# Kernel tuning notes

Measured on AMD Instinct MI355X. Metric: run time of the kernel, lower is better.

## Reference

```python
import jax, jax.numpy as jnp
import numpy as np

N_EXPERTS = 8
TOP_K = 2
W_SCALE = 0.02


def setup_inputs() -> dict:
    key = jax.random.key(0)
    ks = jax.random.split(key, 4)
    S, B, D, F = 2048, 2, 1024, 4096
    x = jax.random.normal(ks[0], (S, B, D), dtype=jnp.float32)
    gate_w = jax.random.normal(ks[1], (D, N_EXPERTS), dtype=jnp.float32) * W_SCALE
    gate_b = jnp.zeros((N_EXPERTS,), dtype=jnp.float32)
    w1 = jax.random.normal(ks[2], (N_EXPERTS, D, F), dtype=jnp.float32) * W_SCALE
    b1 = jnp.zeros((N_EXPERTS, F), dtype=jnp.float32)
    w2 = jax.random.normal(ks[3], (N_EXPERTS, F, D), dtype=jnp.float32) * W_SCALE
    b2 = jnp.zeros((N_EXPERTS, D), dtype=jnp.float32)
    return {"x": x, "gate_w": gate_w, "gate_b": gate_b,
            "w1": w1, "b1": b1, "w2": w2, "b2": b2}


def reference(x, gate_w, gate_b, w1, b1, w2, b2):
    # gate logits: [S, B, E]
    logits = jnp.einsum('sbd,de->sbe', x, gate_w) + gate_b
    top_w, top_idx = jax.lax.top_k(logits, TOP_K)            # [S,B,K]
    # softmax over the top-k logits in float32 (matches dtype=torch.float)
    probs = jax.nn.softmax(top_w.astype(jnp.float32), axis=-1)
    # dense combine weights [S, B, E]: zero for non-selected experts
    comb = jnp.sum(jax.nn.one_hot(top_idx, N_EXPERTS, dtype=probs.dtype)
                   * probs[..., None], axis=-2)
    out = jnp.zeros_like(x)
    for e in range(N_EXPERTS):  # fixed small structural loop over experts
        h = jax.nn.relu(jnp.einsum('sbd,df->sbf', x, w1[e]) + b1[e])
        y = jnp.einsum('sbf,fd->sbd', h, w2[e]) + b2[e]
        out = out + comb[..., e:e + 1].astype(x.dtype) * y
    return out
```

## Files before the change

kernel.cpp:

```cpp
#include <hip/hip_runtime.h>
#include <stdint.h>

#define T_TOK 4096
#define D_DIM 1024
#define F_DIM 4096
#define NEXP 8
#define BM 128
#define BN 128
#define BK 32
#define CAP 9216
#define MT_MAX (CAP / BM)

typedef __attribute__((ext_vector_type(8))) short short8;
typedef __attribute__((ext_vector_type(4))) float f4;
typedef __attribute__((ext_vector_type(4))) unsigned short us4;

#define WS_SBASE   64
#define WS_TBASE   96
#define WS_TOPI    256
#define WS_TOPP    (WS_TOPI + T_TOK*2*4)
#define WS_PSLOT   (WS_TOPP + T_TOK*2*4)
#define WS_XG      102400
#define WS_H       (WS_XG + (size_t)CAP*D_DIM*2)
#define WS_Y       (WS_H + (size_t)CAP*F_DIM*2)
#define WS_WT      (WS_Y + (size_t)CAP*D_DIM*2)

__device__ __forceinline__ unsigned short f2bf(float f) {
    union { float f; uint32_t u; } c; c.f = f;
    uint32_t r = c.u + 0x7FFFu + ((c.u >> 16) & 1u);
    return (unsigned short)(r >> 16);
}
__device__ __forceinline__ float bf2f(unsigned short h) {
    union { uint32_t u; float f; } c; c.u = ((uint32_t)h) << 16;
    return c.f;
}

__global__ __launch_bounds__(256) void gate_kernel(
    const float* __restrict__ x, const float* __restrict__ gw,
    const float* __restrict__ gb,
    int* __restrict__ top_idx, float* __restrict__ top_p)
{
    int lane = threadIdx.x & 63;
    int t = blockIdx.x * 4 + (threadIdx.x >> 6);
    const float* xr = x + (size_t)t * D_DIM;
    float acc[8] = {0.f,0.f,0.f,0.f,0.f,0.f,0.f,0.f};
    for (int i = 0; i < 16; ++i) {
        int d = lane + i * 64;
        float xv = xr[d];
        const float* g = gw + d * 8;
        #pragma unroll
        for (int e = 0; e < 8; ++e) acc[e] += xv * g[e];
    }
    #pragma unroll
    for (int e = 0; e < 8; ++e) {
        #pragma unroll
        for (int off = 32; off > 0; off >>= 1)
            acc[e] += __shfl_xor(acc[e], off, 64);
    }
    if (lane == 0) {
        float l[8];
        #pragma unroll
        for (int e = 0; e < 8; ++e) l[e] = acc[e] + gb[e];
        int i0 = 0; float m0 = l[0];
        #pragma unroll
        for (int e = 1; e < 8; ++e) if (l[e] > m0) { m0 = l[e]; i0 = e; }
        int i1 = -1; float m1 = -3.4e38f;
        #pragma unroll
        for (int e = 0; e < 8; ++e) if (e != i0 && l[e] > m1) { m1 = l[e]; i1 = e; }
        float p0 = 1.f / (1.f + expf(m1 - m0));
        top_idx[t*2]   = i0; top_idx[t*2+1] = i1;
        top_p[t*2]     = p0; top_p[t*2+1]   = 1.f - p0;
    }
}

__global__ __launch_bounds__(256) void plan_kernel(
    const int* __restrict__ top_idx, int* __restrict__ sbase,
    int* __restrict__ tbase, int* __restrict__ pslot)
{
    __shared__ int woff[4][8];
    __shared__ int sb_s[8];
    int t = threadIdx.x, wv = t >> 6, lane = t & 63;
    int base = t * 32;

    int h[8] = {0,0,0,0,0,0,0,0};
    for (int i = 0; i < 32; ++i) {
        int e = top_idx[base + i];
        #pragma unroll
        for (int ee = 0; ee < 8; ++ee) h[ee] += (e == ee) ? 1 : 0;
    }
    int inc[8];
    #pragma unroll
    for (int ee = 0; ee < 8; ++ee) {
        int v = h[ee];
        #pragma unroll
        for (int off = 1; off < 64; off <<= 1) {
            int n = __shfl_up(v, off, 64);
            if (lane >= off) v += n;
        }
        inc[ee] = v;
    }
    if (lane == 63) {
        #pragma unroll
        for (int ee = 0; ee < 8; ++ee) woff[wv][ee] = inc[ee];
    }
    __syncthreads();
    if (t == 0) {
        int cnt[8];
        #pragma unroll
        for (int ee = 0; ee < 8; ++ee) {
            int s = 0;
            #pragma unroll
            for (int w = 0; w < 4; ++w) { int v = woff[w][ee]; woff[w][ee] = s; s += v; }
            cnt[ee] = s;
        }
        int b = 0, tb0 = 0;
        tbase[0] = 0;
        #pragma unroll
        for (int e = 0; e < 8; ++e) {
            sb_s[e] = b; sbase[e] = b;
            int mt = (cnt[e] + BM - 1) / BM;
            b += mt * BM; tb0 += mt;
            tbase[e + 1] = tb0;
        }
    }
    __syncthreads();
    int run[8];
    #pragma unroll
    for (int ee = 0; ee < 8; ++ee)
        run[ee] = sb_s[ee] + woff[wv][ee] + inc[ee] - h[ee];
    for (int i = 0; i < 32; ++i) {
        int e = top_idx[base + i];
        int slot = 0;
        #pragma unroll
        for (int ee = 0; ee < 8; ++ee) slot += (e == ee) ? run[ee] : 0;
        pslot[base + i] = slot;
        #pragma unroll
        for (int ee = 0; ee < 8; ++ee) run[ee] += (e == ee) ? 1 : 0;
    }
}

__global__ __launch_bounds__(256) void gather_kernel(
    const float* __restrict__ x, const int* __restrict__ pslot,
    uint16_t* __restrict__ xg)
{
    int t = blockIdx.x;
    int s0 = pslot[2*t], s1 = pslot[2*t + 1];
    int i = threadIdx.x;
    f4 v = ((const f4*)(x + (size_t)t * D_DIM))[i];
    us4 o;
    o.x = f2bf(v[0]); o.y = f2bf(v[1]); o.z = f2bf(v[2]); o.w = f2bf(v[3]);
    *(us4*)(xg + (size_t)s0 * D_DIM + i * 4) = o;
    *(us4*)(xg + (size_t)s1 * D_DIM + i * 4) = o;
}

__global__ __launch_bounds__(512) void convT_kernel(
    const float* __restrict__ W, uint16_t* __restrict__ WT, int K, int N)
{
    __shared__ float ts[64][65];
    int e = blockIdx.z;
    int n0 = blockIdx.x * 64, k0 = blockIdx.y * 64;
    const float* src = W + (size_t)e * K * N + (size_t)k0 * N + n0;
    int t = threadIdx.x;
    int kk = t >> 3, j = t & 7;
    f4 v0 = *(const f4*)(src + (size_t)kk * N + j * 8);
    f4 v1 = *(const f4*)(src + (size_t)kk * N + j * 8 + 4);
    #pragma unroll
    for (int i = 0; i < 4; ++i) ts[j*8 + i][kk] = v0[i];
    #pragma unroll
    for (int i = 0; i < 4; ++i) ts[j*8 + 4 + i][kk] = v1[i];
    __syncthreads();
    int nn = t >> 3;
    short8 o;
    #pragma unroll
    for (int i = 0; i < 8; ++i) o[i] = (short)f2bf(ts[nn][j*8 + i]);
    *(short8*)(WT + (size_t)e * N * K + (size_t)(n0 + nn) * K + k0 + j * 8) = o;
}

template<bool RELU>
__global__ __launch_bounds__(256, 3) void moe_gemm3(
    const uint16_t* __restrict__ A, const uint16_t* __restrict__ Bt,
    const float* __restrict__ bias, uint16_t* __restrict__ Cc,
    const int* __restrict__ tbase, const int* __restrict__ sbase,
    int K, int N, int NT)
{
    __shared__ uint16_t As3[3][BM][BK];
    __shared__ uint16_t Bs3[3][BN][BK];

    int nwg = gridDim.x;
    int lin = blockIdx.x;
    int wg = (lin & 7) * (nwg >> 3) + (lin >> 3);
    int q = wg >> 2;
    int nt = q % NT;
    int mt = (wg & 3) + (q / NT) * 4;

    if (mt >= tbase[8]) return;
    int e = 0;
    while (mt >= tbase[e + 1]) ++e;
    int row0 = sbase[e] + (mt - tbase[e]) * BM;
    int n0 = nt * BN;
    const uint16_t* Be = Bt + (size_t)e * N * K + (size_t)n0 * K;

    int tid = threadIdx.x;
    int wid = tid >> 6, lane = tid & 63;
    int wrow = (wid >> 1) * 64, wcol = (wid & 1) * 64;

    f4 acc[4][4] = {};

    int ovb = tid * 16;
    int rowA[2], koffA[2];
    #pragma unroll
    for (int j = 0; j < 2; ++j) {
        int ov = ovb + j * 4096;
        int row = ov >> 6;
        int cb  = (ov >> 4) & 3;
        rowA[j]  = row;
        koffA[j] = (cb ^ ((row >> 1) & 3)) << 3;
    }

    int abyte[4], bbyte[4];
    #pragma unroll
    for (int m = 0; m < 4; ++m) {
        int r = wrow + m * 16 + (lane & 15);
        abyte[m] = r * 64 + ((((lane >> 4) ^ ((r >> 1) & 3))) << 4);
    }
    #pragma unroll
    for (int n = 0; n < 4; ++n) {
        int c = wcol + n * 16 + (lane & 15);
        bbyte[n] = c * 64 + ((((lane >> 4) ^ ((c >> 1) & 3))) << 4);
    }
    const char* As0 = (const char*)&As3[0][0][0];
    const char* Bs0 = (const char*)&Bs3[0][0][0];

    auto STAGE = [&](int buf, int kt) {
        #pragma unroll
        for (int j = 0; j < 2; ++j) {
            const uint16_t* gpA = A + (size_t)(row0 + rowA[j]) * K + kt + koffA[j];
            __builtin_amdgcn_global_load_lds(
                (const __attribute__((address_space(1))) void*)gpA,
                (__attribute__((address_space(3))) void*)((char*)&As3[buf][0][0] + ovb + j * 4096),
                16, 0, 0);
            const uint16_t* gpB = Be + (size_t)rowA[j] * K + kt + koffA[j];
            __builtin_amdgcn_global_load_lds(
                (const __attribute__((address_space(1))) void*)gpB,
                (__attribute__((address_space(3))) void*)((char*)&Bs3[buf][0][0] + ovb + j * 4096),
                16, 0, 0);
        }
    };

    int nkt = K / BK;
    STAGE(0, 0);
    STAGE(1, BK);
    asm volatile("s_waitcnt vmcnt(4)" ::: "memory");
    __builtin_amdgcn_s_barrier();

    int buf = 0;
    for (int t = 0; t < nkt; ++t) {
        int cb = buf * 8192;
        short8 af[4], bfr[4];
        #pragma unroll
        for (int m = 0; m < 4; ++m) af[m] = *(const short8*)(As0 + cb + abyte[m]);
        #pragma unroll
        for (int n = 0; n < 4; ++n) bfr[n] = *(const short8*)(Bs0 + cb + bbyte[n]);

        bool stg = (t + 2) < nkt;
        if (stg) {
            int b2 = buf + 2; if (b2 >= 3) b2 -= 3;
            STAGE(b2, (t + 2) * BK);
        }

        #pragma unroll
        for (int m = 0; m < 4; ++m)
            #pragma unroll
            for (int n = 0; n < 4; ++n)
                acc[m][n] = __builtin_amdgcn_mfma_f32_16x16x32_bf16(
                    af[m], bfr[n], acc[m][n], 0, 0, 0);

        if (stg) asm volatile("s_waitcnt vmcnt(4)" ::: "memory");
        else     asm volatile("s_waitcnt vmcnt(0)" ::: "memory");
        __builtin_amdgcn_s_barrier();
        buf = (buf + 1 == 3) ? 0 : buf + 1;
    }

    #pragma unroll
    for (int n = 0; n < 4; ++n) {
        int c = wcol + n * 16 + (lane & 15);
        float bv = bias[(size_t)e * N + n0 + c];
        #pragma unroll
        for (int m = 0; m < 4; ++m) {
            int rb = wrow + m * 16 + (lane >> 4) * 4;
            #pragma unroll
            for (int r = 0; r < 4; ++r) {
                float v = acc[m][n][r] + bv;
                if (RELU) v = fmaxf(v, 0.f);
                Cc[(size_t)(row0 + rb + r) * N + n0 + c] = f2bf(v);
            }
        }
    }
}

__global__ __launch_bounds__(256) void combine_kernel(
    const uint16_t* __restrict__ Y, const int* __restrict__ pair_slot,
    const float* __restrict__ top_p, float* __restrict__ out)
{
    int t = blockIdx.x;
    int s0 = pair_slot[t*2], s1 = pair_slot[t*2+1];
    float p0 = top_p[t*2],  p1 = top_p[t*2+1];
    int i = threadIdx.x * 4;
    us4 a = *(const us4*)(Y + (size_t)s0 * D_DIM + i);
    us4 b = *(const us4*)(Y + (size_t)s1 * D_DIM + i);
    f4 o;
    o[0] = p0 * bf2f(a.x) + p1 * bf2f(b.x);
    o[1] = p0 * bf2f(a.y) + p1 * bf2f(b.y);
    o[2] = p0 * bf2f(a.z) + p1 * bf2f(b.z);
    o[3] = p0 * bf2f(a.w) + p1 * bf2f(b.w);
    *(f4*)(out + (size_t)t * D_DIM + i) = o;
}

extern "C" void kernel_launch(void* const* d_in, const int* in_sizes, int n_in,
                              void* d_out, int out_size, void* d_ws, size_t ws_size,
                              hipStream_t stream)
{
    const float* x  = (const float*)d_in[0];
    const float* gw = (const float*)d_in[1];
    const float* gb = (const float*)d_in[2];
    const float* w1 = (const float*)d_in[3];
    const float* b1 = (const float*)d_in[4];
    const float* w2 = (const float*)d_in[5];
    const float* b2 = (const float*)d_in[6];
    float* out = (float*)d_out;

    char* ws = (char*)d_ws;
    int*   sbase = (int*)(ws + WS_SBASE);
    int*   tbase = (int*)(ws + WS_TBASE);
    int*   topi  = (int*)(ws + WS_TOPI);
    float* topp  = (float*)(ws + WS_TOPP);
    int*   pslot = (int*)(ws + WS_PSLOT);
    uint16_t* xg = (uint16_t*)(ws + WS_XG);
    uint16_t* H  = (uint16_t*)(ws + WS_H);
    uint16_t* Y  = (uint16_t*)(ws + WS_Y);
    uint16_t* WT = (uint16_t*)(ws + WS_WT);

    gate_kernel<<<T_TOK / 4, 256, 0, stream>>>(x, gw, gb, topi, topp);
    plan_kernel<<<1, 256, 0, stream>>>(topi, sbase, tbase, pslot);
    gather_kernel<<<T_TOK, 256, 0, stream>>>(x, pslot, xg);

    convT_kernel<<<dim3(F_DIM/64, D_DIM/64, NEXP), 512, 0, stream>>>(w1, WT, D_DIM, F_DIM);
    moe_gemm3<true ><<<MT_MAX * (F_DIM / BN), 256, 0, stream>>>(
        xg, WT, b1, H, tbase, sbase, D_DIM, F_DIM, F_DIM / BN);
    convT_kernel<<<dim3(D_DIM/64, F_DIM/64, NEXP), 512, 0, stream>>>(w2, WT, F_DIM, D_DIM);
    moe_gemm3<false><<<MT_MAX * (D_DIM / BN), 256, 0, stream>>>(
        H, WT, b2, Y, tbase, sbase, F_DIM, D_DIM, D_DIM / BN);

    combine_kernel<<<T_TOK, 256, 0, stream>>>(Y, pslot, topp, out);
}
```

Baseline: 299.1 us.

## Use 256-row tiles for first expert GEMM and reuse gather buffer for Y

Adds a new moe_gemm5 kernel with 256x128 output tiles (8x4 MFMA accumulators per wave) for the up-projection, so each weight tile loaded into LDS is reused across twice as many rows. The plan kernel now pads each expert's rows to a multiple of 256 and emits separate tile bases for the 256- and 128-row GEMMs. Capacity grows, and Y aliases the xg buffer to save workspace. The larger tiles raise register and LDS pressure and add padding waste per expert.

```diff
diff --git a/kernel.cpp b/kernel.cpp
--- a/kernel.cpp
+++ b/kernel.cpp
@@ -8,8 +8,9 @@
 #define BM 128
 #define BN 128
 #define BK 32
-#define CAP 9216
-#define MT_MAX (CAP / BM)
+#define CAP 10240
+#define MT256 (CAP / 256)
+#define MT128 (CAP / 128)
 
 typedef __attribute__((ext_vector_type(8))) short short8;
 typedef __attribute__((ext_vector_type(4))) float f4;
@@ -17,13 +18,13 @@
 
 #define WS_SBASE   64
 #define WS_TBASE   96
+#define WS_TB128   160
 #define WS_TOPI    256
 #define WS_TOPP    (WS_TOPI + T_TOK*2*4)
 #define WS_PSLOT   (WS_TOPP + T_TOK*2*4)
 #define WS_XG      102400
 #define WS_H       (WS_XG + (size_t)CAP*D_DIM*2)
-#define WS_Y       (WS_H + (size_t)CAP*F_DIM*2)
-#define WS_WT      (WS_Y + (size_t)CAP*D_DIM*2)
+#define WS_WT      (WS_H + (size_t)CAP*F_DIM*2)
 
 __device__ __forceinline__ unsigned short f2bf(float f) {
     union { float f; uint32_t u; } c; c.f = f;
@@ -75,7 +76,8 @@
 
 __global__ __launch_bounds__(256) void plan_kernel(
     const int* __restrict__ top_idx, int* __restrict__ sbase,
-    int* __restrict__ tbase, int* __restrict__ pslot)
+    int* __restrict__ tbase256, int* __restrict__ tbase128,
+    int* __restrict__ pslot)
 {
     __shared__ int woff[4][8];
     __shared__ int sb_s[8];
@@ -113,14 +115,17 @@
             for (int w = 0; w < 4; ++w) { int v = woff[w][ee]; woff[w][ee] = s; s += v; }
             cnt[ee] = s;
         }
-        int b = 0, tb0 = 0;
-        tbase[0] = 0;
+        int b = 0, t2 = 0, t1 = 0;
+        tbase256[0] = 0; tbase128[0] = 0;
         #pragma unroll
         for (int e = 0; e < 8; ++e) {
             sb_s[e] = b; sbase[e] = b;
-            int mt = (cnt[e] + BM - 1) / BM;
-            b += mt * BM; tb0 += mt;
-            tbase[e + 1] = tb0;
+            int m2 = (cnt[e] + 255) / 256;
+            b  += m2 * 256;
+            t2 += m2;
+            t1 += m2 * 2;
+            tbase256[e + 1] = t2;
+            tbase128[e + 1] = t1;
         }
     }
     __syncthreads();
@@ -288,6 +293,132 @@
         #pragma unroll
         for (int m = 0; m < 4; ++m) {
             int rb = wrow + m * 16 + (lane >> 4) * 4;
+            #pragma unroll
+            for (int r = 0; r < 4; ++r) {
+                float v = acc[m][n][r] + bv;
+                if (RELU) v = fmaxf(v, 0.f);
+                Cc[(size_t)(row0 + rb + r) * N + n0 + c] = f2bf(v);
+            }
+        }
+    }
+}
+
+template<bool RELU>
+__global__ __launch_bounds__(256, 2) void moe_gemm5(
+    const uint16_t* __restrict__ A, const uint16_t* __restrict__ Bt,
+    const float* __restrict__ bias, uint16_t* __restrict__ Cc,
+    const int* __restrict__ tbase, const int* __restrict__ sbase,
+    int K, int N, int NT)
+{
+    __shared__ uint16_t As3[3][256][BK];
+    __shared__ uint16_t Bs3[3][BN][BK];
+
+    int nwg = gridDim.x;
+    int lin = blockIdx.x;
+    int wg = (lin & 7) * (nwg >> 3) + (lin >> 3);
+    int q = wg >> 2;
+    int nt = q % NT;
+    int mt = (wg & 3) + (q / NT) * 4;
+
+    if (mt >= tbase[8]) return;
+    int e = 0;
+    while (mt >= tbase[e + 1]) ++e;
+    int row0 = sbase[e] + (mt - tbase[e]) * 256;
+    int n0 = nt * BN;
+    const uint16_t* Be = Bt + (size_t)e * N * K + (size_t)n0 * K;
+
+    int tid = threadIdx.x;
+    int wid = tid >> 6, lane = tid & 63;
+    int wr = wid >> 1, wc = wid & 1;
+    int lq = lane >> 4, lr = lane & 15;
+
+    f4 acc[8][4] = {};
+
+    int ovb = tid * 16;
+    int rowS[4], koffS[4];
+    #pragma unroll
+    for (int j = 0; j < 4; ++j) {
+        int ov = ovb + j * 4096;
+        int row = ov >> 6;
+        int cb  = (ov >> 4) & 3;
+        rowS[j]  = row;
+        koffS[j] = (cb ^ ((row >> 1) & 3)) << 3;
+    }
+
+    int abyte[8], bbyte[4];
+    #pragma unroll
+    for (int m = 0; m < 8; ++m) {
+        int r = wr * 128 + m * 16 + lr;
+        abyte[m] = r * 64 + (((lq ^ ((r >> 1) & 3))) << 4);
+    }
+    #pragma unroll
+    for (int n = 0; n < 4; ++n) {
+        int c = wc * 64 + n * 16 + lr;
+        bbyte[n] = c * 64 + (((lq ^ ((c >> 1) & 3))) << 4);
+    }
+    const char* As0 = (const char*)&As3[0][0][0];
+    const char* Bs0 = (const char*)&Bs3[0][0][0];
+
+    auto STAGE = [&](int buf, int kt) {
+        #pragma unroll
+        for (int j = 0; j < 4; ++j) {
+            const uint16_t* gpA = A + (size_t)(row0 + rowS[j]) * K + kt + koffS[j];
+            __builtin_amdgcn_global_load_lds(
+                (const __attribute__((address_space(1))) void*)gpA,
+                (__attribute__((address_space(3))) void*)((char*)&As3[buf][0][0] + ovb + j * 4096),
+                16, 0, 0);
+        }
+        #pragma unroll
+        for (int j = 0; j < 2; ++j) {
+            const uint16_t* gpB = Be + (size_t)rowS[j] * K + kt + koffS[j];
+            __builtin_amdgcn_global_load_lds(
+                (const __attribute__((address_space(1))) void*)gpB,
+                (__attribute__((address_space(3))) void*)((char*)&Bs3[buf][0][0] + ovb + j * 4096),
+                16, 0, 0);
+        }
+    };
+
+    int nkt = K / BK;
+    STAGE(0, 0);
+    STAGE(1, BK);
+    asm volatile("s_waitcnt vmcnt(6)" ::: "memory");
+    __builtin_amdgcn_s_barrier();
+
+    int buf = 0;
+    for (int t = 0; t < nkt; ++t) {
+        int cba = buf * 16384, cbb = buf * 8192;
+        short8 af[8], bfr[4];
+        #pragma unroll
+        for (int m = 0; m < 8; ++m) af[m] = *(const short8*)(As0 + cba + abyte[m]);
+        #pragma unroll
+        for (int n = 0; n < 4; ++n) bfr[n] = *(const short8*)(Bs0 + cbb + bbyte[n]);
+
+        bool stg = (t + 2) < nkt;
+        if (stg) {
+            int b2 = buf + 2; if (b2 >= 3) b2 -= 3;
+            STAGE(b2, (t + 2) * BK);
+        }
+
+        #pragma unroll
+        for (int m = 0; m < 8; ++m)
+            #pragma unroll
+            for (int n = 0; n < 4; ++n)
+                acc[m][n] = __builtin_amdgcn_mfma_f32_16x16x32_bf16(
+                    af[m], bfr[n], acc[m][n], 0, 0, 0);
+
+        if (stg) asm volatile("s_waitcnt vmcnt(6)" ::: "memory");
+        else     asm volatile("s_waitcnt vmcnt(0)" ::: "memory");
+        __builtin_amdgcn_s_barrier();
+        buf = (buf + 1 == 3) ? 0 : buf + 1;
+    }
+
+    #pragma unroll
+    for (int n = 0; n < 4; ++n) {
+        int c = wc * 64 + n * 16 + lr;
+        float bv = bias[(size_t)e * N + n0 + c];
+        #pragma unroll
+        for (int m = 0; m < 8; ++m) {
+            int rb = wr * 128 + m * 16 + lq * 4;
             #pragma unroll
             for (int r = 0; r < 4; ++r) {
                 float v = acc[m][n][r] + bv;
@@ -331,25 +462,26 @@
 
     char* ws = (char*)d_ws;
     int*   sbase = (int*)(ws + WS_SBASE);
-    int*   tbase = (int*)(ws + WS_TBASE);
+    int*   tb256 = (int*)(ws + WS_TBASE);
+    int*   tb128 = (int*)(ws + WS_TB128);
     int*   topi  = (int*)(ws + WS_TOPI);
     float* topp  = (float*)(ws + WS_TOPP);
     int*   pslot = (int*)(ws + WS_PSLOT);
     uint16_t* xg = (uint16_t*)(ws + WS_XG);
     uint16_t* H  = (uint16_t*)(ws + WS_H);
-    uint16_t* Y  = (uint16_t*)(ws + WS_Y);
+    uint16_t* Y  = xg;
     uint16_t* WT = (uint16_t*)(ws + WS_WT);
 
     gate_kernel<<<T_TOK / 4, 256, 0, stream>>>(x, gw, gb, topi, topp);
-    plan_kernel<<<1, 256, 0, stream>>>(topi, sbase, tbase, pslot);
+    plan_kernel<<<1, 256, 0, stream>>>(topi, sbase, tb256, tb128, pslot);
     gather_kernel<<<T_TOK, 256, 0, stream>>>(x, pslot, xg);
 
     convT_kernel<<<dim3(F_DIM/64, D_DIM/64, NEXP), 512, 0, stream>>>(w1, WT, D_DIM, F_DIM);
-    moe_gemm3<true ><<<MT_MAX * (F_DIM / BN), 256, 0, stream>>>(
-        xg, WT, b1, H, tbase, sbase, D_DIM, F_DIM, F_DIM / BN);
+    moe_gemm5<true ><<<MT256 * (F_DIM / BN), 256, 0, stream>>>(
+        xg, WT, b1, H, tb256, sbase, D_DIM, F_DIM, F_DIM / BN);
     convT_kernel<<<dim3(D_DIM/64, F_DIM/64, NEXP), 512, 0, stream>>>(w2, WT, F_DIM, D_DIM);
-    moe_gemm3<false><<<MT_MAX * (D_DIM / BN), 256, 0, stream>>>(
-        H, WT, b2, Y, tbase, sbase, F_DIM, D_DIM, D_DIM / BN);
+    moe_gemm3<false><<<MT128 * (D_DIM / BN), 256, 0, stream>>>(
+        H, WT, b2, Y, tb128, sbase, F_DIM, D_DIM, D_DIM / BN);
 
     combine_kernel<<<T_TOK, 256, 0, stream>>>(Y, pslot, topp, out);
 }
```

New measurement: 307.8 us. 2.9% more time.
